# Optimization experiments

Hardware: AMD Instinct MI355X
Metric: run time of the kernel (lower is better)

## Reference

```python
import jax, jax.numpy as jnp
import numpy as np

# Gemma-2B style config
B, S, HID = 2, 2048, 2048
H, KH, D = 8, 1, 256          # query heads, kv heads, head_dim
THETA = 10000.0


def setup_inputs() -> dict:
    key = jax.random.key(0)
    ks = jax.random.split(key, 6)
    s = 0.02  # init scale for weights
    return {
        "hidden_states": jax.random.normal(ks[0], (B, S, HID), dtype=jnp.float32),
        "attention_mask": jnp.zeros((B, S), dtype=jnp.float32),  # additive mask over kv axis
        "position_ids": jnp.broadcast_to(jnp.arange(S, dtype=jnp.int32), (B, S)),
        "Wq": jax.random.normal(ks[1], (H * D, HID), dtype=jnp.float32) * s,
        "bq": jnp.zeros((H * D,), dtype=jnp.float32),
        "Wk": jax.random.normal(ks[2], (KH * D, HID), dtype=jnp.float32) * s,
        "bk": jnp.zeros((KH * D,), dtype=jnp.float32),
        "Wv": jax.random.normal(ks[3], (KH * D, HID), dtype=jnp.float32) * s,
        "bv": jnp.zeros((KH * D,), dtype=jnp.float32),
        "Wo": jax.random.normal(ks[4], (HID, H * D), dtype=jnp.float32) * s,
        "bo": jnp.zeros((HID,), dtype=jnp.float32),
    }


def _rope(x, position_ids):
    # x: [b, s, h, d]; rotate-half RoPE per head, computed in fp32 as in the module.
    half = D // 2
    inv_freq = 1.0 / (THETA ** (jnp.arange(0, D, 2, dtype=jnp.float32) / D))  # [d/2]
    freqs = position_ids.astype(jnp.float32)[:, :, None] * inv_freq            # [b, s, d/2]
    cos = jnp.cos(freqs)[:, :, None, :]  # [b, s, 1, d/2]
    sin = jnp.sin(freqs)[:, :, None, :]
    x1, x2 = x[..., :half], x[..., half:]
    return jnp.concatenate([cos * x1 - sin * x2, sin * x1 + cos * x2], axis=-1).astype(x.dtype)


def reference(hidden_states, attention_mask, position_ids, Wq, bq, Wk, bk, Wv, bv, Wo, bo):
    b, s, _ = hidden_states.shape
    q = (hidden_states @ Wq.T + bq).reshape(b, s, H, D)
    k = (hidden_states @ Wk.T + bk).reshape(b, s, KH, D)
    v = (hidden_states @ Wv.T + bv).reshape(b, s, KH, D)
    q = _rope(q, position_ids)
    k = _rope(k, position_ids)
    # GQA: broadcast the KV heads across query-head groups
    groups = H // KH
    k = jnp.repeat(k, groups, axis=2)  # [b, s, H, D]
    v = jnp.repeat(v, groups, axis=2)
    scores = jnp.einsum('bnhd,bmhd->bhnm', q, k) * (D ** -0.5)  # [b, H, s, s]
    scores = scores + attention_mask[:, None, None, :]
    attn = jax.nn.softmax(scores, axis=-1)  # dropout p=0.0 -> identity
    out = jnp.einsum('bhnm,bmhd->bnhd', attn, v).reshape(b, s, H * D)
    out = out @ Wo.T + bo
    return (out, attn)
```

## Files before the change

kernel.cpp:

```cpp
#include <hip/hip_runtime.h>

#define B_ 2
#define S_ 2048
#define HID_ 2048
#define H_ 8
#define D_ 256
#define NQKV 2560

typedef unsigned short u16;
typedef __attribute__((ext_vector_type(8))) short bf16x8;
typedef __attribute__((ext_vector_type(4))) float f32x4;

__device__ __forceinline__ u16 f2b(float x) {
    unsigned u = __float_as_uint(x);
    unsigned rb = (u >> 16) & 1u;
    u += 0x7fffu + rb;
    return (u16)(u >> 16);
}

__device__ __forceinline__ void load_lds16(const u16* g, u16* l) {
    __builtin_amdgcn_global_load_lds(
        (const __attribute__((address_space(1))) void*)g,
        (__attribute__((address_space(3))) void*)l, 16, 0, 0);
}

__global__ __launch_bounds__(256) void cvt_bf16(const float* __restrict__ in,
                                                u16* __restrict__ out, int n) {
    int i = (blockIdx.x * 256 + threadIdx.x) * 4;
    if (i >= n) return;
    float4 f = *(const float4*)(in + i);
    union { u16 u[4]; uint2 v; } pk;
    pk.u[0] = f2b(f.x); pk.u[1] = f2b(f.y); pk.u[2] = f2b(f.z); pk.u[3] = f2b(f.w);
    *(uint2*)(out + i) = pk.v;
}

__global__ __launch_bounds__(256) void concat_bias(const float* __restrict__ bq,
                                                   const float* __restrict__ bk,
                                                   const float* __restrict__ bv,
                                                   float* __restrict__ dst) {
    int i = blockIdx.x * 256 + threadIdx.x;
    if (i >= NQKV) return;
    float v;
    if (i < H_ * D_) v = bq[i];
    else if (i < H_ * D_ + D_) v = bk[i - H_ * D_];
    else v = bv[i - H_ * D_ - D_];
    dst[i] = v;
}

__global__ __launch_bounds__(256) void rope_kernel(const float* __restrict__ x,
                                                   int rowStride, int colOff,
                                                   const int* __restrict__ pos_ids,
                                                   u16* __restrict__ out, int nHeads) {
    int idx = blockIdx.x * 256 + threadIdx.x;
    int d   = idx & 127;
    int tmp = idx >> 7;
    int h   = tmp % nHeads;
    int n   = tmp / nHeads;
    int pos = pos_ids[n];
    float ang = (float)pos * expf(-(float)d * (9.210340371976184f / 128.0f));
    float s, c;
    sincosf(ang, &s, &c);
    size_t src = (size_t)n * rowStride + colOff + (size_t)h * D_;
    float x1 = x[src + d], x2 = x[src + d + 128];
    size_t dst = ((size_t)n * nHeads + h) * D_;
    out[dst + d]       = f2b(c * x1 - s * x2);
    out[dst + d + 128] = f2b(s * x1 + c * x2);
}

__global__ __launch_bounds__(256) void transpose_v(const float* __restrict__ v,
                                                   int rowStride, int colOff,
                                                   u16* __restrict__ vT) {
    __shared__ float t[32][33];
    int b = blockIdx.z;
    int s0 = blockIdx.x * 32, d0 = blockIdx.y * 32;
    int tx = threadIdx.x, ty = threadIdx.y;
#pragma unroll
    for (int i = 0; i < 4; ++i)
        t[ty + i * 8][tx] = v[((size_t)b * S_ + s0 + ty + i * 8) * rowStride + colOff + d0 + tx];
    __syncthreads();
#pragma unroll
    for (int i = 0; i < 4; ++i)
        vT[(size_t)b * D_ * S_ + (size_t)(d0 + ty + i * 8) * S_ + s0 + tx] = f2b(t[tx][ty + i * 8]);
}

__global__ __launch_bounds__(256, 2) void score_softmax(
    const u16* __restrict__ q_b, const u16* __restrict__ k_b,
    const float* __restrict__ mask, float* __restrict__ attn,
    u16* __restrict__ attn_b) {
    __shared__ __align__(16) u16 qs[16 * 256];
    __shared__ __align__(16) u16 ks[64 * 256];
    __shared__ float redm[4][16], reds[4][16];

    const int z = blockIdx.z;
    const int bb = z >> 3, hh = z & 7;
    const int n0 = blockIdx.x * 16;
    const int tid = threadIdx.x;
    const int lane = tid & 63, wave = tid >> 6;
    const int l15 = lane & 15, quad = lane >> 4;

    const u16* qsrc = q_b + (((size_t)bb * S_ + n0) * H_ + hh) * D_;
#pragma unroll
    for (int i = 0; i < 2; ++i) {
        int c = i * 256 + tid;
        int row = c >> 5, sg = c & 31;
        int g = sg ^ (row & 7);
        load_lds16(qsrc + (size_t)row * (H_ * D_) + g * 8,
                   qs + (size_t)(i * 256 + wave * 64) * 8);
    }

    const u16* kbase = k_b + (size_t)bb * S_ * D_;
#pragma unroll
    for (int j = 0; j < 8; ++j) {
        int c = j * 256 + tid;
        int row = c >> 5, sg = c & 31;
        int g = sg ^ (row & 7);
        load_lds16(kbase + (size_t)row * D_ + g * 8,
                   ks + (size_t)(j * 256 + wave * 64) * 8);
    }

    f32x4 acc[32];
#pragma unroll
    for (int ct = 0; ct < 32; ++ct)
#pragma unroll
        for (int r = 0; r < 4; ++r) acc[ct][r] = 0.f;

    __syncthreads();

    bf16x8 av[8];
#pragma unroll
    for (int kk = 0; kk < 8; ++kk)
        av[kk] = *(const bf16x8*)&qs[l15 * 256 + (((kk * 4 + quad) ^ (l15 & 7)) * 8)];

#pragma unroll
    for (int t = 0; t < 32; ++t) {
        bf16x8 bv[8];
        const int rb = wave * 16 + l15;
#pragma unroll
        for (int kk = 0; kk < 8; ++kk)
            bv[kk] = *(const bf16x8*)&ks[rb * 256 + (((kk * 4 + quad) ^ (rb & 7)) * 8)];
#pragma unroll
        for (int kk = 0; kk < 8; ++kk)
            acc[t] = __builtin_amdgcn_mfma_f32_16x16x32_bf16(av[kk], bv[kk], acc[t], 0, 0, 0);
        if (t < 31) {
            __syncthreads();
#pragma unroll
            for (int j = 0; j < 8; ++j) {
                int c = j * 256 + tid;
                int row = c >> 5, sg = c & 31;
                int g = sg ^ (row & 7);
                load_lds16(kbase + (size_t)((t + 1) * 64 + row) * D_ + g * 8,
                           ks + (size_t)(j * 256 + wave * 64) * 8);
            }
            __syncthreads();
        }
    }

    const float sc = 0.0625f;
    const float* maskb = mask + (size_t)bb * S_ + wave * 16 + l15;
    float mx[4] = {-3.4e38f, -3.4e38f, -3.4e38f, -3.4e38f};
#pragma unroll
    for (int ct = 0; ct < 32; ++ct) {
        float mkv = maskb[ct * 64];
#pragma unroll
        for (int r = 0; r < 4; ++r) {
            float xv = acc[ct][r] * sc + mkv;
            acc[ct][r] = xv;
            mx[r] = fmaxf(mx[r], xv);
        }
    }
#pragma unroll
    for (int off = 1; off < 16; off <<= 1)
#pragma unroll
        for (int r = 0; r < 4; ++r) mx[r] = fmaxf(mx[r], __shfl_xor(mx[r], off));
    if (l15 == 0) {
#pragma unroll
        for (int r = 0; r < 4; ++r) redm[wave][quad * 4 + r] = mx[r];
    }
    __syncthreads();
    float fm[4], sm[4];
#pragma unroll
    for (int r = 0; r < 4; ++r) {
        int rw = quad * 4 + r;
        fm[r] = fmaxf(fmaxf(redm[0][rw], redm[1][rw]),
                      fmaxf(redm[2][rw], redm[3][rw]));
        sm[r] = 0.f;
    }
#pragma unroll
    for (int ct = 0; ct < 32; ++ct)
#pragma unroll
        for (int r = 0; r < 4; ++r) {
            float e = expf(acc[ct][r] - fm[r]);
            acc[ct][r] = e;
            sm[r] += e;
        }
#pragma unroll
    for (int off = 1; off < 16; off <<= 1)
#pragma unroll
        for (int r = 0; r < 4; ++r) sm[r] += __shfl_xor(sm[r], off);
    if (l15 == 0) {
#pragma unroll
        for (int r = 0; r < 4; ++r) reds[wave][quad * 4 + r] = sm[r];
    }
    __syncthreads();

    size_t obase = ((size_t)(bb * H_ + hh) * S_ + n0 + quad * 4) * S_
                 + wave * 16 + l15;
#pragma unroll
    for (int r = 0; r < 4; ++r) {
        int rw = quad * 4 + r;
        float inv = 1.f / (reds[0][rw] + reds[1][rw] + reds[2][rw] + reds[3][rw]);
        float* ao = attn + obase + (size_t)r * S_;
#pragma unroll
        for (int ct = 0; ct < 32; ++ct) {
            float p = acc[ct][r] * inv;
            ao[ct * 64] = p;
            acc[ct][r] = p;
        }
    }
    if (attn_b) {
        u16* ab = attn_b + obase;
#pragma unroll
        for (int r = 0; r < 4; ++r) {
            u16* abr = ab + (size_t)r * S_;
#pragma unroll
            for (int ct = 0; ct < 32; ++ct) abr[ct * 64] = f2b(acc[ct][r]);
        }
    }
}

#define TILE_M 128
#define TILE_N 128
#define TILE_K 32

template <bool C_IS_BF16>
__global__ __launch_bounds__(256, 2) void gemm_async(
    const u16* __restrict__ Ap, const u16* __restrict__ Bp, void* __restrict__ Cp,
    const float* __restrict__ bias, int lda, int ldb, int ldc, int K,
    long sAb, long sAh, long sBb, long sBh, long sCb, long sCh, int numH) {
    __shared__ __align__(16) u16 As[TILE_M * TILE_K];
    __shared__ __align__(16) u16 Bs[TILE_N * TILE_K];

    int z = blockIdx.z;
    int bb = z / numH, hh = z % numH;
    const u16* Ab = Ap + (long)bb * sAb + (long)hh * sAh;
    const u16* Bb = Bp + (long)bb * sBb + (long)hh * sBh;
    long cOff = (long)bb * sCb + (long)hh * sCh;

    const int m0 = blockIdx.y * TILE_M;
    const int n0 = blockIdx.x * TILE_N;
    const int tid = threadIdx.x;
    const int lane = tid & 63, wave = tid >> 6;
    const int l15 = lane & 15, quad = lane >> 4;
    const int waveM = wave >> 1, waveN = wave & 1;

    f32x4 acc[4][4];
#pragma unroll
    for (int mt = 0; mt < 4; ++mt)
#pragma unroll
        for (int nt = 0; nt < 4; ++nt)
#pragma unroll
            for (int r = 0; r < 4; ++r) acc[mt][nt][r] = 0.f;

    int rowS[2], colS[2];
    u16 *lA[2], *lB[2];
#pragma unroll
    for (int i = 0; i < 2; ++i) {
        int c = i * 256 + tid;
        rowS[i] = c >> 2;
        colS[i] = (((c & 3) ^ ((rowS[i] >> 1) & 3)) * 8);
        lA[i] = As + (size_t)(i * 256 + wave * 64) * 8;
        lB[i] = Bs + (size_t)(i * 256 + wave * 64) * 8;
    }

    for (int k0 = 0; k0 < K; k0 += TILE_K) {
#pragma unroll
        for (int i = 0; i < 2; ++i) {
            load_lds16(Ab + (size_t)(m0 + rowS[i]) * lda + k0 + colS[i], lA[i]);
            load_lds16(Bb + (size_t)(n0 + rowS[i]) * ldb + k0 + colS[i], lB[i]);
        }
        __syncthreads();

        bf16x8 av[4], bv[4];
#pragma unroll
        for (int t = 0; t < 4; ++t) {
            int ra = waveM * 64 + t * 16 + l15;
            av[t] = *(bf16x8*)&As[ra * TILE_K + ((quad ^ ((ra >> 1) & 3)) * 8)];
            int rb = waveN * 64 + t * 16 + l15;
            bv[t] = *(bf16x8*)&Bs[rb * TILE_K + ((quad ^ ((rb >> 1) & 3)) * 8)];
        }
#pragma unroll
        for (int mt = 0; mt < 4; ++mt)
#pragma unroll
            for (int nt = 0; nt < 4; ++nt)
                acc[mt][nt] = __builtin_amdgcn_mfma_f32_16x16x32_bf16(av[mt], bv[nt],
                                                                      acc[mt][nt], 0, 0, 0);
        __syncthreads();
    }

#pragma unroll
    for (int mt = 0; mt < 4; ++mt) {
        int row = m0 + waveM * 64 + mt * 16 + quad * 4;
#pragma unroll
        for (int nt = 0; nt < 4; ++nt) {
            int col = n0 + waveN * 64 + nt * 16 + l15;
            float bia = bias ? bias[col] : 0.f;
#pragma unroll
            for (int r = 0; r < 4; ++r) {
                float val = acc[mt][nt][r] + bia;
                if constexpr (C_IS_BF16)
                    ((u16*)Cp)[cOff + (size_t)(row + r) * ldc + col] = f2b(val);
                else
                    ((float*)Cp)[cOff + (size_t)(row + r) * ldc + col] = val;
            }
        }
    }
}

#define LDSK 40
__global__ __launch_bounds__(256, 2) void gemm_slow_f32a(
    const float* __restrict__ Ap, const u16* __restrict__ Bp, u16* __restrict__ Cp,
    int lda, int ldb, int ldc, int K,
    long sAb, long sAh, long sBb, long sBh, long sCb, long sCh, int numH) {
    __shared__ __align__(16) u16 As[TILE_M * LDSK];
    __shared__ __align__(16) u16 Bs[TILE_N * LDSK];
    int z = blockIdx.z;
    int bb = z / numH, hh = z % numH;
    const float* Af = Ap + (long)bb * sAb + (long)hh * sAh;
    const u16* Bb = Bp + (long)bb * sBb + (long)hh * sBh;
    long cOff = (long)bb * sCb + (long)hh * sCh;
    const int m0 = blockIdx.y * TILE_M, n0 = blockIdx.x * TILE_N;
    const int tid = threadIdx.x;
    const int lane = tid & 63, wave = tid >> 6;
    const int l15 = lane & 15, quad = lane >> 4;
    const int waveM = wave >> 1, waveN = wave & 1;
    f32x4 acc[4][4];
#pragma unroll
    for (int mt = 0; mt < 4; ++mt)
#pragma unroll
        for (int nt = 0; nt < 4; ++nt)
#pragma unroll
            for (int r = 0; r < 4; ++r) acc[mt][nt][r] = 0.f;
    for (int k0 = 0; k0 < K; k0 += TILE_K) {
#pragma unroll
        for (int i = 0; i < 2; ++i) {
            int c = tid + i * 256;
            int row = c >> 2, col = (c & 3) * 8;
            const float* src = Af + (size_t)(m0 + row) * lda + k0 + col;
            float4 f0 = *(const float4*)src;
            float4 f1 = *(const float4*)(src + 4);
            union { u16 u[8]; uint4 v; } pk;
            pk.u[0] = f2b(f0.x); pk.u[1] = f2b(f0.y); pk.u[2] = f2b(f0.z); pk.u[3] = f2b(f0.w);
            pk.u[4] = f2b(f1.x); pk.u[5] = f2b(f1.y); pk.u[6] = f2b(f1.z); pk.u[7] = f2b(f1.w);
            *(uint4*)&As[row * LDSK + col] = pk.v;
            *(uint4*)&Bs[row * LDSK + col] =
                *(const uint4*)(Bb + (size_t)(n0 + row) * ldb + k0 + col);
        }
        __syncthreads();
        bf16x8 av[4], bv[4];
#pragma unroll
        for (int t = 0; t < 4; ++t) {
            av[t] = *(bf16x8*)&As[(waveM * 64 + t * 16 + l15) * LDSK + quad * 8];
            bv[t] = *(bf16x8*)&Bs[(waveN * 64 + t * 16 + l15) * LDSK + quad * 8];
        }
#pragma unroll
        for (int mt = 0; mt < 4; ++mt)
#pragma unroll
            for (int nt = 0; nt < 4; ++nt)
                acc[mt][nt] = __builtin_amdgcn_mfma_f32_16x16x32_bf16(av[mt], bv[nt],
                                                                      acc[mt][nt], 0, 0, 0);
        __syncthreads();
    }
#pragma unroll
    for (int mt = 0; mt < 4; ++mt) {
        int row = m0 + waveM * 64 + mt * 16 + quad * 4;
#pragma unroll
        for (int nt = 0; nt < 4; ++nt) {
            int col = n0 + waveN * 64 + nt * 16 + l15;
#pragma unroll
            for (int r = 0; r < 4; ++r)
                Cp[cOff + (size_t)(row + r) * ldc + col] = f2b(acc[mt][nt][r]);
        }
    }
}

extern "C" void kernel_launch(void* const* d_in, const int* in_sizes, int n_in,
                              void* d_out, int out_size, void* d_ws, size_t ws_size,
                              hipStream_t stream) {
    const float* hs   = (const float*)d_in[0];
    const float* mask = (const float*)d_in[1];
    const int*   pos  = (const int*)d_in[2];
    const float* Wq = (const float*)d_in[3];
    const float* bq = (const float*)d_in[4];
    const float* Wk = (const float*)d_in[5];
    const float* bk = (const float*)d_in[6];
    const float* Wv = (const float*)d_in[7];
    const float* bv = (const float*)d_in[8];
    const float* Wo = (const float*)d_in[9];
    const float* bo = (const float*)d_in[10];

    float* out  = (float*)d_out;
    float* attn = (float*)d_out + (size_t)B_ * S_ * HID_;

    char* ws = (char*)d_ws;
    size_t need = 0;
    u16* hs_b    = (u16*)(ws);          need += (size_t)B_ * S_ * HID_ * 2;
    u16* Wqkv_b  = (u16*)(ws + need);   need += (size_t)NQKV * HID_ * 2;
    u16* Wo_b    = (u16*)(ws + need);   need += (size_t)HID_ * H_ * D_ * 2;
    float* qkv_f = (float*)(ws + need); need += (size_t)B_ * S_ * NQKV * 4;
    u16* q_b     = (u16*)(ws + need);   need += (size_t)B_ * S_ * H_ * D_ * 2;
    u16* k_b     = (u16*)(ws + need);   need += (size_t)B_ * S_ * D_ * 2;
    u16* vT_b    = (u16*)(ws + need);   need += (size_t)B_ * D_ * S_ * 2;
    float* bqkv  = (float*)(ws + need); need += (size_t)NQKV * 4 + 4096;
    need &= ~(size_t)255;
    u16* attn_b  = (u16*)(ws + need);
    size_t need_big = need + (size_t)B_ * H_ * S_ * S_ * 2;
    bool big = ws_size >= need_big;
    u16* ctx_b = hs_b;

    cvt_bf16<<<dim3((B_ * S_ * HID_) / 1024), 256, 0, stream>>>(hs, hs_b, B_ * S_ * HID_);
    cvt_bf16<<<dim3((H_ * D_ * HID_) / 1024), 256, 0, stream>>>(Wq, Wqkv_b, H_ * D_ * HID_);
    cvt_bf16<<<dim3((D_ * HID_) / 1024), 256, 0, stream>>>(Wk, Wqkv_b + (size_t)H_ * D_ * HID_, D_ * HID_);
    cvt_bf16<<<dim3((D_ * HID_) / 1024), 256, 0, stream>>>(Wv, Wqkv_b + (size_t)(H_ * D_ + D_) * HID_, D_ * HID_);
    cvt_bf16<<<dim3((HID_ * H_ * D_) / 1024), 256, 0, stream>>>(Wo, Wo_b, HID_ * H_ * D_);
    concat_bias<<<dim3((NQKV + 255) / 256), 256, 0, stream>>>(bq, bk, bv, bqkv);

    gemm_async<false><<<dim3(NQKV / TILE_N, (B_ * S_) / TILE_M, 1), 256, 0, stream>>>(
        hs_b, Wqkv_b, qkv_f, bqkv, HID_, HID_, NQKV, HID_,
        0, 0, 0, 0, 0, 0, 1);

    rope_kernel<<<dim3((B_ * S_ * H_ * 128) / 256), 256, 0, stream>>>(
        qkv_f, NQKV, 0, pos, q_b, H_);
    rope_kernel<<<dim3((B_ * S_ * 1 * 128) / 256), 256, 0, stream>>>(
        qkv_f, NQKV, H_ * D_, pos, k_b, 1);
    transpose_v<<<dim3(S_ / 32, D_ / 32, B_), dim3(32, 8), 0, stream>>>(
        qkv_f, NQKV, H_ * D_ + D_, vT_b);

    score_softmax<<<dim3(S_ / 16, 1, B_ * H_), 256, 0, stream>>>(
        q_b, k_b, mask, attn, big ? attn_b : nullptr);

    if (big) {
        gemm_async<true><<<dim3(D_ / TILE_N, S_ / TILE_M, B_ * H_), 256, 0, stream>>>(
            attn_b, vT_b, ctx_b, nullptr, S_, S_, H_ * D_, S_,
            (long)H_ * S_ * S_, (long)S_ * S_,
            (long)D_ * S_, 0,
            (long)S_ * H_ * D_, D_,
            H_);
    } else {
        gemm_slow_f32a<<<dim3(D_ / TILE_N, S_ / TILE_M, B_ * H_), 256, 0, stream>>>(
            attn, vT_b, ctx_b, S_, S_, H_ * D_, S_,
            (long)H_ * S_ * S_, (long)S_ * S_,
            (long)D_ * S_, 0,
            (long)S_ * H_ * D_, D_,
            H_);
    }

    gemm_async<false><<<dim3(HID_ / TILE_N, (B_ * S_) / TILE_M, 1), 256, 0, stream>>>(
        ctx_b, Wo_b, out, bo, H_ * D_, H_ * D_, HID_, H_ * D_,
        0, 0, 0, 0, 0, 0, 1);
}
```

Baseline: 741.9 us.

## Double-buffer K tiles in LDS and use exp2 in softmax

The score kernel now uses two LDS buffers for K tiles. It issues the asynchronous global-to-LDS load for tile t+1 before running the MFMAs on tile t, and keeps one barrier per iteration instead of two, so K loads can overlap compute. The softmax exponent is rewritten as exp2f of the difference scaled by log2(e), which maps onto the native exp2 instruction. This doubles K-tile LDS use to 64 KB per block (72 KB total), which could limit occupancy. Correctness relies on the barrier waiting for the outstanding LDS-direct loads.

```diff
diff --git a/kernel.cpp b/kernel.cpp
--- a/kernel.cpp
+++ b/kernel.cpp
@@ -88,7 +88,7 @@
     const float* __restrict__ mask, float* __restrict__ attn,
     u16* __restrict__ attn_b) {
     __shared__ __align__(16) u16 qs[16 * 256];
-    __shared__ __align__(16) u16 ks[64 * 256];
+    __shared__ __align__(16) u16 ks[2][64 * 256];
     __shared__ float redm[4][16], reds[4][16];
 
     const int z = blockIdx.z;
@@ -98,25 +98,22 @@
     const int lane = tid & 63, wave = tid >> 6;
     const int l15 = lane & 15, quad = lane >> 4;
 
-    const u16* qsrc = q_b + (((size_t)bb * S_ + n0) * H_ + hh) * D_;
-#pragma unroll
-    for (int i = 0; i < 2; ++i) {
-        int c = i * 256 + tid;
-        int row = c >> 5, sg = c & 31;
-        int g = sg ^ (row & 7);
-        load_lds16(qsrc + (size_t)row * (H_ * D_) + g * 8,
+    const int tr5 = tid >> 5;
+    const int gsw = ((tid & 31) ^ tr5) * 8;
+    const size_t koff = (size_t)tr5 * D_ + gsw;
+
+    const u16* qsrc  = q_b + (((size_t)bb * S_ + n0) * H_ + hh) * D_;
+    const u16* kbase = k_b + (size_t)bb * S_ * D_;
+
+#pragma unroll
+    for (int i = 0; i < 2; ++i)
+        load_lds16(qsrc + (size_t)(i * 8 + tr5) * (H_ * D_) + gsw,
                    qs + (size_t)(i * 256 + wave * 64) * 8);
-    }
-
-    const u16* kbase = k_b + (size_t)bb * S_ * D_;
-#pragma unroll
-    for (int j = 0; j < 8; ++j) {
-        int c = j * 256 + tid;
-        int row = c >> 5, sg = c & 31;
-        int g = sg ^ (row & 7);
-        load_lds16(kbase + (size_t)row * D_ + g * 8,
-                   ks + (size_t)(j * 256 + wave * 64) * 8);
-    }
+
+#pragma unroll
+    for (int j = 0; j < 8; ++j)
+        load_lds16(kbase + (size_t)(j * 8) * D_ + koff,
+                   ks[0] + (size_t)(j * 256 + wave * 64) * 8);
 
     f32x4 acc[32];
 #pragma unroll
@@ -131,28 +128,28 @@
     for (int kk = 0; kk < 8; ++kk)
         av[kk] = *(const bf16x8*)&qs[l15 * 256 + (((kk * 4 + quad) ^ (l15 & 7)) * 8)];
 
+    const int rb = wave * 16 + l15;
+    const int rbo = rb * 256;
+
 #pragma unroll
     for (int t = 0; t < 32; ++t) {
+        if (t < 31) {
+            u16* dst = ks[(t + 1) & 1];
+            const u16* src = kbase + (size_t)((t + 1) * 64) * D_ + koff;
+#pragma unroll
+            for (int j = 0; j < 8; ++j)
+                load_lds16(src + (size_t)(j * 8) * D_,
+                           dst + (size_t)(j * 256 + wave * 64) * 8);
+        }
+        const u16* kst = ks[t & 1];
         bf16x8 bv[8];
-        const int rb = wave * 16 + l15;
 #pragma unroll
         for (int kk = 0; kk < 8; ++kk)
-            bv[kk] = *(const bf16x8*)&ks[rb * 256 + (((kk * 4 + quad) ^ (rb & 7)) * 8)];
+            bv[kk] = *(const bf16x8*)&kst[rbo + (((kk * 4 + quad) ^ (rb & 7)) * 8)];
 #pragma unroll
         for (int kk = 0; kk < 8; ++kk)
             acc[t] = __builtin_amdgcn_mfma_f32_16x16x32_bf16(av[kk], bv[kk], acc[t], 0, 0, 0);
-        if (t < 31) {
-            __syncthreads();
-#pragma unroll
-            for (int j = 0; j < 8; ++j) {
-                int c = j * 256 + tid;
-                int row = c >> 5, sg = c & 31;
-                int g = sg ^ (row & 7);
-                load_lds16(kbase + (size_t)((t + 1) * 64 + row) * D_ + g * 8,
-                           ks + (size_t)(j * 256 + wave * 64) * 8);
-            }
-            __syncthreads();
-        }
+        __syncthreads();
     }
 
     const float sc = 0.0625f;
@@ -177,6 +174,7 @@
         for (int r = 0; r < 4; ++r) redm[wave][quad * 4 + r] = mx[r];
     }
     __syncthreads();
+    const float LOG2E = 1.4426950408889634f;
     float fm[4], sm[4];
 #pragma unroll
     for (int r = 0; r < 4; ++r) {
@@ -189,7 +187,7 @@
     for (int ct = 0; ct < 32; ++ct)
 #pragma unroll
         for (int r = 0; r < 4; ++r) {
-            float e = expf(acc[ct][r] - fm[r]);
+            float e = exp2f((acc[ct][r] - fm[r]) * LOG2E);
             acc[ct][r] = e;
             sm[r] += e;
         }
```

Result: faster. 719.7 us (-3.0%).
